# Kernel tuning notes

Hardware: AMD Instinct MI355X
Metric: run time of the kernel (lower is better)

## Reference

```python
import jax, jax.numpy as jnp
import numpy as np

N_NODES = 50000
LEAKY_SLOPE = 0.2


def _degrees(idx, n):
    d = jax.ops.segment_sum(jnp.ones_like(idx, dtype=jnp.float32), idx, num_segments=n)
    return jnp.clip(d, 1.0)  # DGL clamps zero degrees to 1


def _gcn_layer(x, W, b, src, dst, out_inv_sqrt, in_inv_sqrt):
    # norm='both': h = D_in^{-1/2} A D_out^{-1/2} x, then x @ W + b
    h = x * out_inv_sqrt[:, None]
    agg = jax.ops.segment_sum(jnp.take(h, src, axis=0), dst, num_segments=N_NODES)
    agg = agg * in_inv_sqrt[:, None]
    return agg @ W + b


def setup_inputs() -> dict:
    key = jax.random.key(0)
    k1, k2, k3, k4, k5 = jax.random.split(key, 5)
    E = 800000
    init_emb = jax.random.normal(k1, (N_NODES, 300), dtype=jnp.float32)
    W1 = jax.random.normal(k2, (300, 400), dtype=jnp.float32) * (1.0 / np.sqrt(300.0))
    b1 = jnp.zeros((400,), dtype=jnp.float32)
    W2 = jax.random.normal(k3, (400, 512), dtype=jnp.float32) * (1.0 / np.sqrt(400.0))
    b2 = jnp.zeros((512,), dtype=jnp.float32)
    src = jax.random.randint(k4, (E,), 0, N_NODES, dtype=jnp.int32)
    dst = jax.random.randint(k5, (E,), 0, N_NODES, dtype=jnp.int32)
    return {"init_emb": init_emb, "W1": W1, "b1": b1, "W2": W2, "b2": b2,
            "src": src, "dst": dst}


def reference(init_emb, W1, b1, W2, b2, src, dst):
    out_inv_sqrt = jax.lax.rsqrt(_degrees(src, N_NODES))  # D_out^{-1/2}
    in_inv_sqrt = jax.lax.rsqrt(_degrees(dst, N_NODES))   # D_in^{-1/2}
    x = _gcn_layer(init_emb, W1, b1, src, dst, out_inv_sqrt, in_inv_sqrt)
    x = jnp.where(x >= 0, x, LEAKY_SLOPE * x)  # LeakyReLU(0.2); dropout = identity (eval)
    x = _gcn_layer(x, W2, b2, src, dst, out_inv_sqrt, in_inv_sqrt)
    return x
```

## Files before the change

### kernel.cpp

```cpp
#include <hip/hip_runtime.h>
#include <hip/hip_fp16.h>

#define NN   50000
#define NNP  50048
#define D0   300
#define K1   320
#define N1   400
#define K2   448
#define N2   512
#define NBLK 196

typedef __attribute__((ext_vector_type(8))) short bf16x8;
typedef __attribute__((ext_vector_type(4))) float f32x4;
typedef __attribute__((ext_vector_type(4))) unsigned int u32x4;

__device__ __forceinline__ unsigned short f2bf(float x) {
    union { float f; unsigned u; } v; v.f = x;
    unsigned r = v.u + 0x7fffu + ((v.u >> 16) & 1u);
    return (unsigned short)(r >> 16);
}

__global__ __launch_bounds__(256) void hist_kernel(const int* __restrict__ src,
                                                   const int* __restrict__ dst,
                                                   int* __restrict__ cnt_s,
                                                   int* __restrict__ cnt_d, int E) {
    int e = blockIdx.x * 256 + threadIdx.x;
    if (e < E) {
        atomicAdd(&cnt_s[src[e]], 1);
        atomicAdd(&cnt_d[dst[e]], 1);
    }
}

__global__ __launch_bounds__(256) void scan_blk_kernel(const int* __restrict__ cnt,
                                                       int* __restrict__ offs,
                                                       int* __restrict__ bsum) {
    __shared__ int sh[256];
    int t = threadIdx.x, g = blockIdx.x * 256 + t;
    int v = (g < NN) ? cnt[g] : 0;
    sh[t] = v;
    __syncthreads();
    for (int off = 1; off < 256; off <<= 1) {
        int u = (t >= off) ? sh[t - off] : 0;
        __syncthreads();
        sh[t] += u;
        __syncthreads();
    }
    if (g < NN) offs[g] = sh[t] - v;
    if (t == 255) bsum[blockIdx.x] = sh[255];
}

__global__ __launch_bounds__(256) void scan_top_kernel(const int* __restrict__ bsum,
                                                       int* __restrict__ boff) {
    __shared__ int sh[256];
    int t = threadIdx.x;
    int v = (t < NBLK) ? bsum[t] : 0;
    sh[t] = v;
    __syncthreads();
    for (int off = 1; off < 256; off <<= 1) {
        int u = (t >= off) ? sh[t - off] : 0;
        __syncthreads();
        sh[t] += u;
        __syncthreads();
    }
    if (t < NBLK) boff[t] = sh[t] - v;
}

__global__ __launch_bounds__(256) void scan_fix_kernel(int* __restrict__ offs,
                                                       const int* __restrict__ boff,
                                                       const int* __restrict__ cnt_s,
                                                       const int* __restrict__ cnt_d,
                                                       float* __restrict__ deg_s,
                                                       float* __restrict__ deg_d, int E) {
    int g = blockIdx.x * 256 + threadIdx.x;
    if (g < NN) {
        offs[g] += boff[blockIdx.x];
        deg_s[g] = rsqrtf(fmaxf((float)cnt_s[g], 1.0f));
        deg_d[g] = rsqrtf(fmaxf((float)cnt_d[g], 1.0f));
    }
    if (g == NN) offs[NN] = E;
}

__global__ __launch_bounds__(256) void scatter_kernel(const int* __restrict__ src,
                                                      const int* __restrict__ dst,
                                                      const int* __restrict__ offs,
                                                      int* __restrict__ cursor,
                                                      int* __restrict__ ssrc, int E) {
    int e = blockIdx.x * 256 + threadIdx.x;
    if (e < E) {
        int d = dst[e];
        int pos = atomicAdd(&cursor[d], 1);
        ssrc[offs[d] + pos] = src[e];
    }
}

__global__ __launch_bounds__(256) void embh_kernel(const float* __restrict__ emb,
                                                   const float* __restrict__ deg_s,
                                                   __half* __restrict__ embh) {
    int tid = blockIdx.x * 256 + threadIdx.x;
    const int CPR = K1 / 4;
    const int total = NN * CPR;
    if (tid >= total) return;
    int node = tid / CPR, c = tid - node * CPR;
    int f = 4 * c;
    __half h[4] = {__half(0.f), __half(0.f), __half(0.f), __half(0.f)};
    if (f < D0) {
        float sc = deg_s[node];
        float4 v = *(const float4*)(emb + (size_t)node * D0 + f);
        h[0] = __float2half(v.x * sc); h[1] = __float2half(v.y * sc);
        h[2] = __float2half(v.z * sc); h[3] = __float2half(v.w * sc);
    }
    *(uint2*)(embh + (size_t)node * K1 + f) = *(uint2*)h;
}

__global__ __launch_bounds__(256) void wt_kernel(const float* __restrict__ W1,
                                                 const float* __restrict__ W2,
                                                 unsigned short* __restrict__ T1,
                                                 unsigned short* __restrict__ T2) {
    int tid = blockIdx.x * 256 + threadIdx.x;
    if (tid < K2 * K1) {
        int n = tid / K1, k = tid - n * K1;
        float v = (n < N1 && k < D0) ? W1[k * N1 + n] : 0.f;
        T1[tid] = f2bf(v);
    } else {
        int u = tid - K2 * K1;
        if (u >= N2 * K2) return;
        int n = u / K2, k = u - n * K2;
        float v = (k < N1) ? W2[k * N2 + n] : 0.f;
        T2[u] = f2bf(v);
    }
}

template <int LD, int KP>
__global__ __launch_bounds__(256) void agg_h_kernel(
    const __half* __restrict__ X, const int* __restrict__ offs,
    const int* __restrict__ ssrc, const float* __restrict__ nscale,
    unsigned short* __restrict__ O) {
    constexpr int D8 = LD / 8;
    constexpr int O8 = KP / 8;
    int node = blockIdx.x * 4 + (threadIdx.x >> 6);
    if (node >= NNP) return;
    int l = threadIdx.x & 63;
    bool act = l < D8;
    const uint4* Xq = (const uint4*)X;

    float a[8] = {0.f, 0.f, 0.f, 0.f, 0.f, 0.f, 0.f, 0.f};

#define ACCUM(U) { const __half2* hp = (const __half2*)&(U);                        \
                   float2 f0 = __half22float2(hp[0]), f1 = __half22float2(hp[1]);   \
                   float2 f2 = __half22float2(hp[2]), f3 = __half22float2(hp[3]);   \
                   a[0] += f0.x; a[1] += f0.y; a[2] += f1.x; a[3] += f1.y;          \
                   a[4] += f2.x; a[5] += f2.y; a[6] += f3.x; a[7] += f3.y; }

    if (node < NN) {
        int j = offs[node], end = offs[node + 1];
        for (; j + 8 <= end; j += 8) {
            uint4 u0, u1, u2, u3, u4, u5, u6, u7;
            int s0 = ssrc[j + 0], s1 = ssrc[j + 1], s2 = ssrc[j + 2], s3 = ssrc[j + 3];
            int s4 = ssrc[j + 4], s5 = ssrc[j + 5], s6 = ssrc[j + 6], s7 = ssrc[j + 7];
            if (act) {
                u0 = Xq[(size_t)s0 * D8 + l]; u1 = Xq[(size_t)s1 * D8 + l];
                u2 = Xq[(size_t)s2 * D8 + l]; u3 = Xq[(size_t)s3 * D8 + l];
                u4 = Xq[(size_t)s4 * D8 + l]; u5 = Xq[(size_t)s5 * D8 + l];
                u6 = Xq[(size_t)s6 * D8 + l]; u7 = Xq[(size_t)s7 * D8 + l];
                ACCUM(u0); ACCUM(u1); ACCUM(u2); ACCUM(u3);
                ACCUM(u4); ACCUM(u5); ACCUM(u6); ACCUM(u7);
            }
        }
        for (; j + 2 <= end; j += 2) {
            int s0 = ssrc[j + 0], s1 = ssrc[j + 1];
            if (act) {
                uint4 u0 = Xq[(size_t)s0 * D8 + l];
                uint4 u1 = Xq[(size_t)s1 * D8 + l];
                ACCUM(u0); ACCUM(u1);
            }
        }
        for (; j < end; ++j) {
            int s0 = ssrc[j];
            if (act) { uint4 u0 = Xq[(size_t)s0 * D8 + l]; ACCUM(u0); }
        }
        float ns = nscale[node];
#pragma unroll
        for (int i = 0; i < 8; ++i) a[i] *= ns;
    }
#undef ACCUM

    if (l < O8) {
        unsigned short hv[8];
#pragma unroll
        for (int i = 0; i < 8; ++i) hv[i] = f2bf(a[i]);
        __builtin_nontemporal_store(*(u32x4*)hv, (u32x4*)(O + (size_t)node * KP + 8 * l));
    }
}

template <bool LRELU_SCALE, bool WRITE_HALF>
__global__ __launch_bounds__(256) void gemm_bf16_kernel(
    const unsigned short* __restrict__ A, const unsigned short* __restrict__ BT,
    const float* __restrict__ bias, const float* __restrict__ rs,
    void* __restrict__ Cv, int nbn, int Kpad, int Nvalid, int Cld) {
    __shared__ unsigned short lds[12288];
    const int AOF = 0, BOF = 8192;

    int nwg = (int)gridDim.x, orig = (int)blockIdx.x;
    int q8 = nwg >> 3, r8 = nwg & 7;
    int xc = orig & 7, o8 = orig >> 3;
    int wg = (xc < r8 ? xc * (q8 + 1) : r8 * (q8 + 1) + (xc - r8) * q8) + o8;
    int bn = wg % nbn, bm = wg / nbn;
    int m0 = bm * 128, n0 = bn * 64;

    int t = threadIdx.x, l = t & 63, w = t >> 6;
    int wm = w >> 1, wn = w & 1;

    f32x4 acc[4][2] = {};

    for (int k0 = 0; k0 < Kpad; k0 += 64) {
#pragma unroll
        for (int j = 0; j < 4; ++j) {
            int c = j * 256 + t;
            int r = c >> 3, qs = c & 7;
            size_t goff = (size_t)(m0 + r) * Kpad + k0 + ((qs ^ (r & 7)) << 3);
            int lbase = (j * 256 + w * 64) * 8;
            __builtin_amdgcn_global_load_lds(
                (const __attribute__((address_space(1))) void*)(A + goff),
                (__attribute__((address_space(3))) void*)&lds[AOF + lbase], 16, 0, 0);
        }
#pragma unroll
        for (int j = 0; j < 2; ++j) {
            int c = j * 256 + t;
            int r = c >> 3, qs = c & 7;
            size_t goff = (size_t)(n0 + r) * Kpad + k0 + ((qs ^ (r & 7)) << 3);
            int lbase = (j * 256 + w * 64) * 8;
            __builtin_amdgcn_global_load_lds(
                (const __attribute__((address_space(1))) void*)(BT + goff),
                (__attribute__((address_space(3))) void*)&lds[BOF + lbase], 16, 0, 0);
        }
        __syncthreads();

#pragma unroll
        for (int ks = 0; ks < 2; ++ks) {
            bf16x8 bfr[2];
#pragma unroll
            for (int ni = 0; ni < 2; ++ni) {
                int n = wn * 32 + ni * 16 + (l & 15);
                int slot = ks * 4 + (l >> 4);
                int idx = n * 64 + ((slot ^ (n & 7)) << 3);
                bfr[ni] = *(const bf16x8*)&lds[BOF + idx];
            }
#pragma unroll
            for (int mi = 0; mi < 4; ++mi) {
                int m = wm * 64 + mi * 16 + (l & 15);
                int slot = ks * 4 + (l >> 4);
                int idx = m * 64 + ((slot ^ (m & 7)) << 3);
                bf16x8 afr = *(const bf16x8*)&lds[AOF + idx];
#pragma unroll
                for (int ni = 0; ni < 2; ++ni)
                    acc[mi][ni] = __builtin_amdgcn_mfma_f32_16x16x32_bf16(afr, bfr[ni], acc[mi][ni], 0, 0, 0);
            }
        }
        __syncthreads();
    }

#pragma unroll
    for (int mi = 0; mi < 4; ++mi) {
        int mbase = m0 + wm * 64 + mi * 16 + ((l >> 4) << 2);
#pragma unroll
        for (int q = 0; q < 4; ++q) {
            int m = mbase + q;
            if (m >= NN) continue;
            float scale = LRELU_SCALE ? rs[m] : 1.0f;
#pragma unroll
            for (int ni = 0; ni < 2; ++ni) {
                int n = n0 + wn * 32 + ni * 16 + (l & 15);
                if (n >= Nvalid) continue;
                float v = acc[mi][ni][q] + bias[n];
                if (LRELU_SCALE) { v = v >= 0.f ? v : 0.2f * v; v *= scale; }
                if (WRITE_HALF)
                    ((__half*)Cv)[(size_t)m * Cld + n] = __float2half(v);
                else
                    ((float*)Cv)[(size_t)m * Cld + n] = v;
            }
        }
    }
}

extern "C" void kernel_launch(void* const* d_in, const int* in_sizes, int n_in,
                              void* d_out, int out_size, void* d_ws, size_t ws_size,
                              hipStream_t stream) {
    const float* emb = (const float*)d_in[0];
    const float* W1  = (const float*)d_in[1];
    const float* b1  = (const float*)d_in[2];
    const float* W2  = (const float*)d_in[3];
    const float* b2  = (const float*)d_in[4];
    const int*   src = (const int*)d_in[5];
    const int*   dst = (const int*)d_in[6];
    const int E = in_sizes[5];

    unsigned short* A1   = (unsigned short*)d_ws;
    unsigned short* A2   = A1 + (size_t)NNP * K1;
    __half*         embh = (__half*)A2;
    unsigned short* W1T  = A2 + (size_t)NNP * K2;
    unsigned short* W2T  = W1T + (size_t)K2 * K1;

    __half* h2  = (__half*)d_out;
    float*  out = (float*)d_out;
    char* tail = (char*)d_out + (size_t)NN * N1 * sizeof(__half);
    int* cnt_s  = (int*)tail;
    int* cnt_d  = cnt_s + NN;
    int* cursor = cnt_d + NN;
    int* offs   = cursor + NN;
    int* bsum   = offs + NN + 1;
    int* boff   = bsum + NBLK;
    int* ssrc   = boff + NBLK;
    float* deg_s = (float*)(ssrc + E);
    float* deg_d = deg_s + NN;

    hipMemsetAsync(cnt_s, 0, (size_t)(3 * NN) * sizeof(int), stream);

    hist_kernel<<<(E + 255) / 256, 256, 0, stream>>>(src, dst, cnt_s, cnt_d, E);
    scan_blk_kernel<<<NBLK, 256, 0, stream>>>(cnt_d, offs, bsum);
    scan_top_kernel<<<1, 256, 0, stream>>>(bsum, boff);
    scan_fix_kernel<<<NBLK, 256, 0, stream>>>(offs, boff, cnt_s, cnt_d, deg_s, deg_d, E);
    scatter_kernel<<<(E + 255) / 256, 256, 0, stream>>>(src, dst, offs, cursor, ssrc, E);

    embh_kernel<<<(NN * (K1 / 4) + 255) / 256, 256, 0, stream>>>(emb, deg_s, embh);
    wt_kernel<<<(K2 * K1 + N2 * K2 + 255) / 256, 256, 0, stream>>>(W1, W2, W1T, W2T);

    agg_h_kernel<K1, K1><<<NNP / 4, 256, 0, stream>>>(embh, offs, ssrc, deg_d, A1);

    gemm_bf16_kernel<true, true><<<391 * 7, 256, 0, stream>>>(
        A1, W1T, b1, deg_s, h2, 7, K1, N1, N1);

    agg_h_kernel<N1, K2><<<NNP / 4, 256, 0, stream>>>(h2, offs, ssrc, deg_d, A2);

    gemm_bf16_kernel<false, false><<<391 * 8, 256, 0, stream>>>(
        A2, W2T, b2, nullptr, out, 8, K2, N2, N2);
}
```

Before: 418.8 us.

## Widen GEMM tile to 128x128 and shrink padded embedding stride for gather

Doubles the GEMM N-tile to 128 columns so each workgroup reuses its A tile across more MFMAs and halves the number of A re-reads; W1T is padded to 512 columns to fit. The fp16 embedding buffer stride is reduced from 320 to 304 halves so the first sparse aggregation gathers fewer bytes per edge. The larger tile raises register and LDS use, and the first GEMM now computes more padded columns.

```diff
diff --git a/kernel.cpp b/kernel.cpp
--- a/kernel.cpp
+++ b/kernel.cpp
@@ -4,8 +4,10 @@
 #define NN   50000
 #define NNP  50048
 #define D0   300
+#define K1E  304
 #define K1   320
 #define N1   400
+#define N1P  512
 #define K2   448
 #define N2   512
 #define NBLK 196
@@ -97,7 +99,7 @@
                                                    const float* __restrict__ deg_s,
                                                    __half* __restrict__ embh) {
     int tid = blockIdx.x * 256 + threadIdx.x;
-    const int CPR = K1 / 4;
+    const int CPR = K1E / 4;
     const int total = NN * CPR;
     if (tid >= total) return;
     int node = tid / CPR, c = tid - node * CPR;
@@ -109,7 +111,7 @@
         h[0] = __float2half(v.x * sc); h[1] = __float2half(v.y * sc);
         h[2] = __float2half(v.z * sc); h[3] = __float2half(v.w * sc);
     }
-    *(uint2*)(embh + (size_t)node * K1 + f) = *(uint2*)h;
+    *(uint2*)(embh + (size_t)node * K1E + f) = *(uint2*)h;
 }
 
 __global__ __launch_bounds__(256) void wt_kernel(const float* __restrict__ W1,
@@ -117,12 +119,12 @@
                                                  unsigned short* __restrict__ T1,
                                                  unsigned short* __restrict__ T2) {
     int tid = blockIdx.x * 256 + threadIdx.x;
-    if (tid < K2 * K1) {
+    if (tid < N1P * K1) {
         int n = tid / K1, k = tid - n * K1;
         float v = (n < N1 && k < D0) ? W1[k * N1 + n] : 0.f;
         T1[tid] = f2bf(v);
     } else {
-        int u = tid - K2 * K1;
+        int u = tid - N1P * K1;
         if (u >= N2 * K2) return;
         int n = u / K2, k = u - n * K2;
         float v = (k < N1) ? W2[k * N2 + n] : 0.f;
@@ -197,7 +199,7 @@
     const unsigned short* __restrict__ A, const unsigned short* __restrict__ BT,
     const float* __restrict__ bias, const float* __restrict__ rs,
     void* __restrict__ Cv, int nbn, int Kpad, int Nvalid, int Cld) {
-    __shared__ unsigned short lds[12288];
+    __shared__ unsigned short lds[16384];
     const int AOF = 0, BOF = 8192;
 
     int nwg = (int)gridDim.x, orig = (int)blockIdx.x;
@@ -205,54 +207,47 @@
     int xc = orig & 7, o8 = orig >> 3;
     int wg = (xc < r8 ? xc * (q8 + 1) : r8 * (q8 + 1) + (xc - r8) * q8) + o8;
     int bn = wg % nbn, bm = wg / nbn;
-    int m0 = bm * 128, n0 = bn * 64;
+    int m0 = bm * 128, n0 = bn * 128;
 
     int t = threadIdx.x, l = t & 63, w = t >> 6;
     int wm = w >> 1, wn = w & 1;
 
-    f32x4 acc[4][2] = {};
+    f32x4 acc[4][4] = {};
 
     for (int k0 = 0; k0 < Kpad; k0 += 64) {
 #pragma unroll
         for (int j = 0; j < 4; ++j) {
             int c = j * 256 + t;
             int r = c >> 3, qs = c & 7;
-            size_t goff = (size_t)(m0 + r) * Kpad + k0 + ((qs ^ (r & 7)) << 3);
+            size_t goffA = (size_t)(m0 + r) * Kpad + k0 + ((qs ^ (r & 7)) << 3);
+            size_t goffB = (size_t)(n0 + r) * Kpad + k0 + ((qs ^ (r & 7)) << 3);
             int lbase = (j * 256 + w * 64) * 8;
             __builtin_amdgcn_global_load_lds(
-                (const __attribute__((address_space(1))) void*)(A + goff),
+                (const __attribute__((address_space(1))) void*)(A + goffA),
                 (__attribute__((address_space(3))) void*)&lds[AOF + lbase], 16, 0, 0);
-        }
-#pragma unroll
-        for (int j = 0; j < 2; ++j) {
-            int c = j * 256 + t;
-            int r = c >> 3, qs = c & 7;
-            size_t goff = (size_t)(n0 + r) * Kpad + k0 + ((qs ^ (r & 7)) << 3);
-            int lbase = (j * 256 + w * 64) * 8;
             __builtin_amdgcn_global_load_lds(
-                (const __attribute__((address_space(1))) void*)(BT + goff),
+                (const __attribute__((address_space(1))) void*)(BT + goffB),
                 (__attribute__((address_space(3))) void*)&lds[BOF + lbase], 16, 0, 0);
         }
         __syncthreads();
 
 #pragma unroll
         for (int ks = 0; ks < 2; ++ks) {
-            bf16x8 bfr[2];
-#pragma unroll
-            for (int ni = 0; ni < 2; ++ni) {
-                int n = wn * 32 + ni * 16 + (l & 15);
-                int slot = ks * 4 + (l >> 4);
+            int slot = ks * 4 + (l >> 4);
+            bf16x8 bfr[4];
+#pragma unroll
+            for (int ni = 0; ni < 4; ++ni) {
+                int n = wn * 64 + ni * 16 + (l & 15);
                 int idx = n * 64 + ((slot ^ (n & 7)) << 3);
                 bfr[ni] = *(const bf16x8*)&lds[BOF + idx];
             }
 #pragma unroll
             for (int mi = 0; mi < 4; ++mi) {
                 int m = wm * 64 + mi * 16 + (l & 15);
-                int slot = ks * 4 + (l >> 4);
                 int idx = m * 64 + ((slot ^ (m & 7)) << 3);
                 bf16x8 afr = *(const bf16x8*)&lds[AOF + idx];
 #pragma unroll
-                for (int ni = 0; ni < 2; ++ni)
+                for (int ni = 0; ni < 4; ++ni)
                     acc[mi][ni] = __builtin_amdgcn_mfma_f32_16x16x32_bf16(afr, bfr[ni], acc[mi][ni], 0, 0, 0);
             }
         }
@@ -268,8 +263,8 @@
             if (m >= NN) continue;
             float scale = LRELU_SCALE ? rs[m] : 1.0f;
 #pragma unroll
-            for (int ni = 0; ni < 2; ++ni) {
-                int n = n0 + wn * 32 + ni * 16 + (l & 15);
+            for (int ni = 0; ni < 4; ++ni) {
+                int n = n0 + wn * 64 + ni * 16 + (l & 15);
                 if (n >= Nvalid) continue;
                 float v = acc[mi][ni][q] + bias[n];
                 if (LRELU_SCALE) { v = v >= 0.f ? v : 0.2f * v; v *= scale; }
@@ -298,7 +293,7 @@
     unsigned short* A2   = A1 + (size_t)NNP * K1;
     __half*         embh = (__half*)A2;
     unsigned short* W1T  = A2 + (size_t)NNP * K2;
-    unsigned short* W2T  = W1T + (size_t)K2 * K1;
+    unsigned short* W2T  = W1T + (size_t)N1P * K1;
 
     __half* h2  = (__half*)d_out;
     float*  out = (float*)d_out;
@@ -321,16 +316,16 @@
     scan_fix_kernel<<<NBLK, 256, 0, stream>>>(offs, boff, cnt_s, cnt_d, deg_s, deg_d, E);
     scatter_kernel<<<(E + 255) / 256, 256, 0, stream>>>(src, dst, offs, cursor, ssrc, E);
 
-    embh_kernel<<<(NN * (K1 / 4) + 255) / 256, 256, 0, stream>>>(emb, deg_s, embh);
-    wt_kernel<<<(K2 * K1 + N2 * K2 + 255) / 256, 256, 0, stream>>>(W1, W2, W1T, W2T);
-
-    agg_h_kernel<K1, K1><<<NNP / 4, 256, 0, stream>>>(embh, offs, ssrc, deg_d, A1);
-
-    gemm_bf16_kernel<true, true><<<391 * 7, 256, 0, stream>>>(
-        A1, W1T, b1, deg_s, h2, 7, K1, N1, N1);
+    embh_kernel<<<(NN * (K1E / 4) + 255) / 256, 256, 0, stream>>>(emb, deg_s, embh);
+    wt_kernel<<<(N1P * K1 + N2 * K2 + 255) / 256, 256, 0, stream>>>(W1, W2, W1T, W2T);
+
+    agg_h_kernel<K1E, K1><<<NNP / 4, 256, 0, stream>>>(embh, offs, ssrc, deg_d, A1);
+
+    gemm_bf16_kernel<true, true><<<391 * 4, 256, 0, stream>>>(
+        A1, W1T, b1, deg_s, h2, 4, K1, N1, N1);
 
     agg_h_kernel<N1, K2><<<NNP / 4, 256, 0, stream>>>(h2, offs, ssrc, deg_d, A2);
 
-    gemm_bf16_kernel<false, false><<<391 * 8, 256, 0, stream>>>(
-        A2, W2T, b2, nullptr, out, 8, K2, N2, N2);
-}
+    gemm_bf16_kernel<false, false><<<391 * 4, 256, 0, stream>>>(
+        A2, W2T, b2, nullptr, out, 4, K2, N2, N2);
+}
```

Measured after the change: 441.4 us. 5.4% more time.

## Split feature columns across two blocks and pack two nodes per wavefront in aggregation

Applied to the files above, without the earlier changes.

The aggregation kernel now splits each node's feature row into two column halves handled by different blocks, with each 64-lane wavefront processing two nodes' half-rows. Before, many lanes sat idle, since rows of 40-50 chunks left 14-24 of 64 lanes unused. The layer-1 fp16 embedding row stride also shrinks from 320 to 304 halves to cut padding bytes in the gather. The price is more complex indexing, and the two nodes sharing a wavefront can have different degrees, which causes divergence between the half-waves.

```diff
diff --git a/kernel.cpp b/kernel.cpp
--- a/kernel.cpp
+++ b/kernel.cpp
@@ -4,6 +4,7 @@
 #define NN   50000
 #define NNP  50048
 #define D0   300
+#define K1E  304
 #define K1   320
 #define N1   400
 #define K2   448
@@ -97,7 +98,7 @@
                                                    const float* __restrict__ deg_s,
                                                    __half* __restrict__ embh) {
     int tid = blockIdx.x * 256 + threadIdx.x;
-    const int CPR = K1 / 4;
+    const int CPR = K1E / 4;
     const int total = NN * CPR;
     if (tid >= total) return;
     int node = tid / CPR, c = tid - node * CPR;
@@ -109,7 +110,7 @@
         h[0] = __float2half(v.x * sc); h[1] = __float2half(v.y * sc);
         h[2] = __float2half(v.z * sc); h[3] = __float2half(v.w * sc);
     }
-    *(uint2*)(embh + (size_t)node * K1 + f) = *(uint2*)h;
+    *(uint2*)(embh + (size_t)node * K1E + f) = *(uint2*)h;
 }
 
 __global__ __launch_bounds__(256) void wt_kernel(const float* __restrict__ W1,
@@ -137,10 +138,20 @@
     unsigned short* __restrict__ O) {
     constexpr int D8 = LD / 8;
     constexpr int O8 = KP / 8;
-    int node = blockIdx.x * 4 + (threadIdx.x >> 6);
-    if (node >= NNP) return;
-    int l = threadIdx.x & 63;
-    bool act = l < D8;
+    constexpr int H0 = D8 / 2;
+    constexpr int H1 = O8 - H0;
+
+    int blk = blockIdx.x;
+    int grp = blk >> 3, slot = blk & 7;
+    int half = slot >> 2, sub4 = slot & 3;
+    int w = threadIdx.x >> 6, l = threadIdx.x & 63;
+    const int H = half ? H1 : H0;
+    int nsub = (l >= H) ? 1 : 0;
+    int cl = l - nsub * H;
+    bool lane_act = l < 2 * H;
+    int abs_chunk = half * H0 + cl;
+    bool gath = lane_act && (abs_chunk < D8);
+    int node = grp * 32 + sub4 * 8 + w * 2 + nsub;
     const uint4* Xq = (const uint4*)X;
 
     float a[8] = {0.f, 0.f, 0.f, 0.f, 0.f, 0.f, 0.f, 0.f};
@@ -157,26 +168,26 @@
             uint4 u0, u1, u2, u3, u4, u5, u6, u7;
             int s0 = ssrc[j + 0], s1 = ssrc[j + 1], s2 = ssrc[j + 2], s3 = ssrc[j + 3];
             int s4 = ssrc[j + 4], s5 = ssrc[j + 5], s6 = ssrc[j + 6], s7 = ssrc[j + 7];
-            if (act) {
-                u0 = Xq[(size_t)s0 * D8 + l]; u1 = Xq[(size_t)s1 * D8 + l];
-                u2 = Xq[(size_t)s2 * D8 + l]; u3 = Xq[(size_t)s3 * D8 + l];
-                u4 = Xq[(size_t)s4 * D8 + l]; u5 = Xq[(size_t)s5 * D8 + l];
-                u6 = Xq[(size_t)s6 * D8 + l]; u7 = Xq[(size_t)s7 * D8 + l];
+            if (gath) {
+                u0 = Xq[(size_t)s0 * D8 + abs_chunk]; u1 = Xq[(size_t)s1 * D8 + abs_chunk];
+                u2 = Xq[(size_t)s2 * D8 + abs_chunk]; u3 = Xq[(size_t)s3 * D8 + abs_chunk];
+                u4 = Xq[(size_t)s4 * D8 + abs_chunk]; u5 = Xq[(size_t)s5 * D8 + abs_chunk];
+                u6 = Xq[(size_t)s6 * D8 + abs_chunk]; u7 = Xq[(size_t)s7 * D8 + abs_chunk];
                 ACCUM(u0); ACCUM(u1); ACCUM(u2); ACCUM(u3);
                 ACCUM(u4); ACCUM(u5); ACCUM(u6); ACCUM(u7);
             }
         }
         for (; j + 2 <= end; j += 2) {
             int s0 = ssrc[j + 0], s1 = ssrc[j + 1];
-            if (act) {
-                uint4 u0 = Xq[(size_t)s0 * D8 + l];
-                uint4 u1 = Xq[(size_t)s1 * D8 + l];
+            if (gath) {
+                uint4 u0 = Xq[(size_t)s0 * D8 + abs_chunk];
+                uint4 u1 = Xq[(size_t)s1 * D8 + abs_chunk];
                 ACCUM(u0); ACCUM(u1);
             }
         }
         for (; j < end; ++j) {
             int s0 = ssrc[j];
-            if (act) { uint4 u0 = Xq[(size_t)s0 * D8 + l]; ACCUM(u0); }
+            if (gath) { uint4 u0 = Xq[(size_t)s0 * D8 + abs_chunk]; ACCUM(u0); }
         }
         float ns = nscale[node];
 #pragma unroll
@@ -184,11 +195,12 @@
     }
 #undef ACCUM
 
-    if (l < O8) {
+    if (lane_act) {
         unsigned short hv[8];
 #pragma unroll
         for (int i = 0; i < 8; ++i) hv[i] = f2bf(a[i]);
-        __builtin_nontemporal_store(*(u32x4*)hv, (u32x4*)(O + (size_t)node * KP + 8 * l));
+        __builtin_nontemporal_store(*(u32x4*)hv,
+                                    (u32x4*)(O + (size_t)node * KP + 8 * abs_chunk));
     }
 }
 
@@ -321,15 +333,15 @@
     scan_fix_kernel<<<NBLK, 256, 0, stream>>>(offs, boff, cnt_s, cnt_d, deg_s, deg_d, E);
     scatter_kernel<<<(E + 255) / 256, 256, 0, stream>>>(src, dst, offs, cursor, ssrc, E);
 
-    embh_kernel<<<(NN * (K1 / 4) + 255) / 256, 256, 0, stream>>>(emb, deg_s, embh);
+    embh_kernel<<<(NN * (K1E / 4) + 255) / 256, 256, 0, stream>>>(emb, deg_s, embh);
     wt_kernel<<<(K2 * K1 + N2 * K2 + 255) / 256, 256, 0, stream>>>(W1, W2, W1T, W2T);
 
-    agg_h_kernel<K1, K1><<<NNP / 4, 256, 0, stream>>>(embh, offs, ssrc, deg_d, A1);
+    agg_h_kernel<K1E, K1><<<(NNP / 32) * 8, 256, 0, stream>>>(embh, offs, ssrc, deg_d, A1);
 
     gemm_bf16_kernel<true, true><<<391 * 7, 256, 0, stream>>>(
         A1, W1T, b1, deg_s, h2, 7, K1, N1, N1);
 
-    agg_h_kernel<N1, K2><<<NNP / 4, 256, 0, stream>>>(h2, offs, ssrc, deg_d, A2);
+    agg_h_kernel<N1, K2><<<(NNP / 32) * 8, 256, 0, stream>>>(h2, offs, ssrc, deg_d, A2);
 
     gemm_bf16_kernel<false, false><<<391 * 8, 256, 0, stream>>>(
         A2, W2T, b2, nullptr, out, 8, K2, N2, N2);
```

Result: slower. 441.6 us (+5.4%).

## Store layer-1 activations as FP8 and add FP8 gather-aggregation kernel

Applied to the files above, without the earlier changes.

The first GEMM epilogue now writes the LeakyReLU-scaled hidden activations as FP8 (one byte per element) instead of fp16. A new aggregation kernel gathers these FP8 rows, unpacks them with hardware FP8-to-f32 conversion, and accumulates in fp32 before writing bf16. This halves the bytes moved by the second, gather-heavy aggregation. Separately, the fp16 embedding row pitch shrinks from 320 to 304 to cut padding in the first gather. FP8 storage adds quantization error that may strain accuracy tolerance.

```diff
diff --git a/kernel.cpp b/kernel.cpp
--- a/kernel.cpp
+++ b/kernel.cpp
@@ -4,6 +4,7 @@
 #define NN   50000
 #define NNP  50048
 #define D0   300
+#define K1E  304
 #define K1   320
 #define N1   400
 #define K2   448
@@ -12,6 +13,7 @@
 
 typedef __attribute__((ext_vector_type(8))) short bf16x8;
 typedef __attribute__((ext_vector_type(4))) float f32x4;
+typedef __attribute__((ext_vector_type(2))) float f32x2;
 typedef __attribute__((ext_vector_type(4))) unsigned int u32x4;
 
 __device__ __forceinline__ unsigned short f2bf(float x) {
@@ -97,7 +99,7 @@
                                                    const float* __restrict__ deg_s,
                                                    __half* __restrict__ embh) {
     int tid = blockIdx.x * 256 + threadIdx.x;
-    const int CPR = K1 / 4;
+    const int CPR = K1E / 4;
     const int total = NN * CPR;
     if (tid >= total) return;
     int node = tid / CPR, c = tid - node * CPR;
@@ -109,7 +111,7 @@
         h[0] = __float2half(v.x * sc); h[1] = __float2half(v.y * sc);
         h[2] = __float2half(v.z * sc); h[3] = __float2half(v.w * sc);
     }
-    *(uint2*)(embh + (size_t)node * K1 + f) = *(uint2*)h;
+    *(uint2*)(embh + (size_t)node * K1E + f) = *(uint2*)h;
 }
 
 __global__ __launch_bounds__(256) void wt_kernel(const float* __restrict__ W1,
@@ -192,7 +194,76 @@
     }
 }
 
-template <bool LRELU_SCALE, bool WRITE_HALF>
+__global__ __launch_bounds__(256) void agg_q_kernel(
+    const unsigned char* __restrict__ X, const int* __restrict__ offs,
+    const int* __restrict__ ssrc, const float* __restrict__ nscale,
+    unsigned short* __restrict__ O) {
+    constexpr int D16 = 25;
+    constexpr int OS  = 28;
+    int node = blockIdx.x * 4 + (threadIdx.x >> 6);
+    if (node >= NNP) return;
+    int l = threadIdx.x & 63;
+    bool act = l < D16;
+    const uint4* Xq = (const uint4*)X;
+
+    float a[16];
+#pragma unroll
+    for (int i = 0; i < 16; ++i) a[i] = 0.f;
+
+#define ACCQ(U) { f32x2 p;                                                          \
+    p = __builtin_amdgcn_cvt_pk_f32_fp8((int)(U).x, false); a[0]+=p.x;  a[1]+=p.y;  \
+    p = __builtin_amdgcn_cvt_pk_f32_fp8((int)(U).x, true);  a[2]+=p.x;  a[3]+=p.y;  \
+    p = __builtin_amdgcn_cvt_pk_f32_fp8((int)(U).y, false); a[4]+=p.x;  a[5]+=p.y;  \
+    p = __builtin_amdgcn_cvt_pk_f32_fp8((int)(U).y, true);  a[6]+=p.x;  a[7]+=p.y;  \
+    p = __builtin_amdgcn_cvt_pk_f32_fp8((int)(U).z, false); a[8]+=p.x;  a[9]+=p.y;  \
+    p = __builtin_amdgcn_cvt_pk_f32_fp8((int)(U).z, true);  a[10]+=p.x; a[11]+=p.y; \
+    p = __builtin_amdgcn_cvt_pk_f32_fp8((int)(U).w, false); a[12]+=p.x; a[13]+=p.y; \
+    p = __builtin_amdgcn_cvt_pk_f32_fp8((int)(U).w, true);  a[14]+=p.x; a[15]+=p.y; }
+
+    if (node < NN) {
+        int j = offs[node], end = offs[node + 1];
+        for (; j + 8 <= end; j += 8) {
+            uint4 u0, u1, u2, u3, u4, u5, u6, u7;
+            int s0 = ssrc[j + 0], s1 = ssrc[j + 1], s2 = ssrc[j + 2], s3 = ssrc[j + 3];
+            int s4 = ssrc[j + 4], s5 = ssrc[j + 5], s6 = ssrc[j + 6], s7 = ssrc[j + 7];
+            if (act) {
+                u0 = Xq[(size_t)s0 * D16 + l]; u1 = Xq[(size_t)s1 * D16 + l];
+                u2 = Xq[(size_t)s2 * D16 + l]; u3 = Xq[(size_t)s3 * D16 + l];
+                u4 = Xq[(size_t)s4 * D16 + l]; u5 = Xq[(size_t)s5 * D16 + l];
+                u6 = Xq[(size_t)s6 * D16 + l]; u7 = Xq[(size_t)s7 * D16 + l];
+                ACCQ(u0); ACCQ(u1); ACCQ(u2); ACCQ(u3);
+                ACCQ(u4); ACCQ(u5); ACCQ(u6); ACCQ(u7);
+            }
+        }
+        for (; j + 2 <= end; j += 2) {
+            int s0 = ssrc[j + 0], s1 = ssrc[j + 1];
+            if (act) {
+                uint4 u0 = Xq[(size_t)s0 * D16 + l];
+                uint4 u1 = Xq[(size_t)s1 * D16 + l];
+                ACCQ(u0); ACCQ(u1);
+            }
+        }
+        for (; j < end; ++j) {
+            int s0 = ssrc[j];
+            if (act) { uint4 u0 = Xq[(size_t)s0 * D16 + l]; ACCQ(u0); }
+        }
+        float ns = nscale[node];
+#pragma unroll
+        for (int i = 0; i < 16; ++i) a[i] *= ns;
+    }
+#undef ACCQ
+
+    if (l < OS) {
+        unsigned short hv[16];
+#pragma unroll
+        for (int i = 0; i < 16; ++i) hv[i] = f2bf(a[i]);
+        unsigned short* dst = O + (size_t)node * K2 + 16 * l;
+        __builtin_nontemporal_store(*(u32x4*)hv, (u32x4*)dst);
+        __builtin_nontemporal_store(*(u32x4*)(hv + 8), (u32x4*)(dst + 8));
+    }
+}
+
+template <int OMODE>
 __global__ __launch_bounds__(256) void gemm_bf16_kernel(
     const unsigned short* __restrict__ A, const unsigned short* __restrict__ BT,
     const float* __restrict__ bias, const float* __restrict__ rs,
@@ -266,17 +337,20 @@
         for (int q = 0; q < 4; ++q) {
             int m = mbase + q;
             if (m >= NN) continue;
-            float scale = LRELU_SCALE ? rs[m] : 1.0f;
+            float scale = (OMODE == 1) ? rs[m] : 1.0f;
 #pragma unroll
             for (int ni = 0; ni < 2; ++ni) {
                 int n = n0 + wn * 32 + ni * 16 + (l & 15);
                 if (n >= Nvalid) continue;
                 float v = acc[mi][ni][q] + bias[n];
-                if (LRELU_SCALE) { v = v >= 0.f ? v : 0.2f * v; v *= scale; }
-                if (WRITE_HALF)
-                    ((__half*)Cv)[(size_t)m * Cld + n] = __float2half(v);
-                else
+                if (OMODE == 1) {
+                    v = v >= 0.f ? v : 0.2f * v;
+                    v *= scale;
+                    int pk = __builtin_amdgcn_cvt_pk_fp8_f32(v, v, 0, false);
+                    ((unsigned char*)Cv)[(size_t)m * Cld + n] = (unsigned char)(pk & 0xff);
+                } else {
                     ((float*)Cv)[(size_t)m * Cld + n] = v;
+                }
             }
         }
     }
@@ -300,9 +374,9 @@
     unsigned short* W1T  = A2 + (size_t)NNP * K2;
     unsigned short* W2T  = W1T + (size_t)K2 * K1;
 
-    __half* h2  = (__half*)d_out;
-    float*  out = (float*)d_out;
-    char* tail = (char*)d_out + (size_t)NN * N1 * sizeof(__half);
+    unsigned char* h2  = (unsigned char*)d_out;
+    float*         out = (float*)d_out;
+    char* tail = (char*)d_out + (size_t)NN * N1;
     int* cnt_s  = (int*)tail;
     int* cnt_d  = cnt_s + NN;
     int* cursor = cnt_d + NN;
@@ -321,16 +395,16 @@
     scan_fix_kernel<<<NBLK, 256, 0, stream>>>(offs, boff, cnt_s, cnt_d, deg_s, deg_d, E);
     scatter_kernel<<<(E + 255) / 256, 256, 0, stream>>>(src, dst, offs, cursor, ssrc, E);
 
-    embh_kernel<<<(NN * (K1 / 4) + 255) / 256, 256, 0, stream>>>(emb, deg_s, embh);
+    embh_kernel<<<(NN * (K1E / 4) + 255) / 256, 256, 0, stream>>>(emb, deg_s, embh);
     wt_kernel<<<(K2 * K1 + N2 * K2 + 255) / 256, 256, 0, stream>>>(W1, W2, W1T, W2T);
 
-    agg_h_kernel<K1, K1><<<NNP / 4, 256, 0, stream>>>(embh, offs, ssrc, deg_d, A1);
-
-    gemm_bf16_kernel<true, true><<<391 * 7, 256, 0, stream>>>(
+    agg_h_kernel<K1E, K1><<<NNP / 4, 256, 0, stream>>>(embh, offs, ssrc, deg_d, A1);
+
+    gemm_bf16_kernel<1><<<391 * 7, 256, 0, stream>>>(
         A1, W1T, b1, deg_s, h2, 7, K1, N1, N1);
 
-    agg_h_kernel<N1, K2><<<NNP / 4, 256, 0, stream>>>(h2, offs, ssrc, deg_d, A2);
-
-    gemm_bf16_kernel<false, false><<<391 * 8, 256, 0, stream>>>(
+    agg_q_kernel<<<NNP / 4, 256, 0, stream>>>(h2, offs, ssrc, deg_d, A2);
+
+    gemm_bf16_kernel<0><<<391 * 8, 256, 0, stream>>>(
         A2, W2T, b2, nullptr, out, 8, K2, N2, N2);
 }
```

After: 411.8 us. Within noise of the previous version (-1.7%).
